# Optimization experiments

Hardware: AMD Instinct MI355X
Metric: run time of the kernel (lower is better)

The kernel has to match this reference:

```python
import jax, jax.numpy as jnp
import numpy as np

B, N, S = 4, 4096, 1024
C1, C2, CO, K = 128, 256, 128, 16
BN_EPS = 1e-5


def setup_inputs() -> dict:
    key = jax.random.key(0)
    ks = jax.random.split(key, 8)
    s = 0.05
    return {
        "xyz1": jax.random.normal(ks[0], (B, N, 3), jnp.float32),
        "xyz2": jax.random.normal(ks[1], (B, S, 3), jnp.float32),
        "points1": jax.random.normal(ks[2], (B, C1, N), jnp.float32),
        "points2": jax.random.normal(ks[3], (B, C2, S), jnp.float32),
        # fuse = ConvBNReLU1D(384 -> 128, k=1)
        "fuse_w": jax.random.normal(ks[4], (CO, C1 + C2), jnp.float32) * s,
        "fuse_b": jnp.zeros((CO,), jnp.float32),
        "fuse_gamma": jnp.ones((CO,), jnp.float32),
        "fuse_beta": jnp.zeros((CO,), jnp.float32),
        # LaplacianUnit conv1x1 (128 -> 128) + BN
        "lu_w": jax.random.normal(ks[5], (CO, CO), jnp.float32) * s,
        "lu_b": jnp.zeros((CO,), jnp.float32),
        "lu_gamma": jnp.ones((CO,), jnp.float32),
        "lu_beta": jnp.zeros((CO,), jnp.float32),
    }


def _sqdist(a, b):
    # a: [B,N,3], b: [B,M,3] -> [B,N,M] squared euclidean distance
    return ((a * a).sum(-1)[:, :, None] + (b * b).sum(-1)[:, None, :]
            - 2.0 * jnp.einsum("bnc,bmc->bnm", a, b))


def _batchnorm1d(x, gamma, beta):
    # x: [B,C,N], training-mode BN (batch statistics, biased variance)
    mean = x.mean(axis=(0, 2), keepdims=True)
    var = ((x - mean) ** 2).mean(axis=(0, 2), keepdims=True)
    xn = (x - mean) * jax.lax.rsqrt(var + BN_EPS)
    return xn * gamma[None, :, None] + beta[None, :, None]


def _gather_points(pts, idx):
    # pts: [B,M,C], idx: [B,N,k] int -> [B,N,k,C]
    return jax.vmap(lambda p, i: p[i])(pts, idx)


def _forward(xyz1, xyz2, points1, points2,
             fuse_w, fuse_b, fuse_gamma, fuse_beta,
             lu_w, lu_b, lu_gamma, lu_beta):
    p2 = jnp.swapaxes(points2, 1, 2)  # [B,S,C2]
    # --- 3-point interpolation (note: torch code uses topk default largest=True) ---
    dists = _sqdist(xyz1, xyz2)                    # [B,N,S]
    top_d, idx = jax.lax.top_k(dists, 3)           # largest, descending (faithful)
    dist_recip = 1.0 / (top_d + 1e-8)
    weight = dist_recip / dist_recip.sum(axis=2, keepdims=True)  # [B,N,3]
    interp = (_gather_points(p2, idx) * weight[..., None]).sum(axis=2)  # [B,N,C2]
    # --- concat skip + fuse conv1x1 + BN + ReLU ---
    new_pts = jnp.concatenate([jnp.swapaxes(points1, 1, 2), interp], axis=-1)  # [B,N,C1+C2]
    x = jnp.einsum("oc,bnc->bon", fuse_w, new_pts) + fuse_b[None, :, None]     # [B,CO,N]
    x = jax.nn.relu(_batchnorm1d(x, fuse_gamma, fuse_beta))
    # --- LaplacianUnit: KNN(k=16) neighbor-sum minus self ---
    d_self = _sqdist(xyz1, xyz1)                   # [B,N,N]
    _, knn_idx = jax.lax.top_k(-d_self, K)         # k smallest distances -> [B,N,K]
    xt = jnp.swapaxes(x, 1, 2)                     # [B,N,CO]
    nbr_sum = _gather_points(xt, knn_idx).sum(axis=2)  # [B,N,CO]
    dx = jnp.swapaxes(nbr_sum, 1, 2) - x           # [B,CO,N]
    h = jnp.einsum("oc,bcn->bon", lu_w, dx) + lu_b[None, :, None]
    h = _batchnorm1d(jax.nn.relu(h), lu_gamma, lu_beta)  # bn(relu(conv(dx))), faithful order
    return x + h


def reference(xyz1, xyz2, points1, points2,
              fuse_w, fuse_b, fuse_gamma, fuse_beta,
              lu_w, lu_b, lu_gamma, lu_beta):
    return _forward(xyz1, xyz2, points1, points2,
                    fuse_w, fuse_b, fuse_gamma, fuse_beta,
                    lu_w, lu_b, lu_gamma, lu_beta)
```

## Files before the change

### kernel.cpp

```cpp
#include <hip/hip_runtime.h>
#include <cfloat>

#define NB 4
#define NN 4096
#define NS 1024
#define NC1 128
#define NC2 256
#define NCO 128
#define NCC 384
#define NK 16
#define KCHUNK 2048
#define KCAP 160
#define KPAD 161


__device__ __forceinline__ float norm3_np(float x, float y, float z) {
  return __fadd_rn(__fadd_rn(__fmul_rn(x, x), __fmul_rn(y, y)), __fmul_rn(z, z));
}

__device__ __forceinline__ float sqdist_np(float nq, float ns,
                                           float qx, float qy, float qz,
                                           float sx, float sy, float sz) {
  float dot = __fadd_rn(__fadd_rn(__fmul_rn(qx, sx), __fmul_rn(qy, sy)),
                        __fmul_rn(qz, sz));
  return __fsub_rn(__fadd_rn(nq, ns), __fmul_rn(2.0f, dot));
}

__global__ void transpose_k(const float* __restrict__ in, float* __restrict__ out,
                            int rows_in, int cols_in, long in_bs, long out_bs, int out_rs) {
  __shared__ float tile[32][33];
  const int b = blockIdx.z;
  const int c0 = blockIdx.x * 32, r0 = blockIdx.y * 32;
  const float* ib = in + (long)b * in_bs;
  float* ob = out + (long)b * out_bs;
#pragma unroll
  for (int k = 0; k < 32; k += 8) {
    tile[threadIdx.y + k][threadIdx.x] =
        ib[(long)(r0 + threadIdx.y + k) * cols_in + c0 + threadIdx.x];
  }
  __syncthreads();
#pragma unroll
  for (int k = 0; k < 32; k += 8) {
    ob[(long)(c0 + threadIdx.y + k) * out_rs + (r0 + threadIdx.x)] =
        tile[threadIdx.x][threadIdx.y + k];
  }
}

__global__ __launch_bounds__(256) void interp_top3_k(const float* __restrict__ xyz1,
                                                     const float* __restrict__ xyz2,
                                                     float* __restrict__ wW,
                                                     int* __restrict__ wIdx) {
  __shared__ float sx[NS], sy[NS], sz[NS], sn[NS];
  __shared__ float md[256 * 3];
  __shared__ int mi[256 * 3];
  const int b = blockIdx.y;
  const int tid = threadIdx.x;
  for (int i = tid; i < NS; i += 256) {
    long base = ((long)b * NS + i) * 3;
    float x = xyz2[base], y = xyz2[base + 1], z = xyz2[base + 2];
    sx[i] = x; sy[i] = y; sz[i] = z;
    sn[i] = norm3_np(x, y, z);
  }
  __syncthreads();
  const int q = (blockIdx.x << 5) + (tid >> 3);
  const int lane = tid & 7;
  long qb = ((long)b * NN + q) * 3;
  const float qx = xyz1[qb], qy = xyz1[qb + 1], qz = xyz1[qb + 2];
  const float nq = norm3_np(qx, qy, qz);
  float bd[3] = {-FLT_MAX, -FLT_MAX, -FLT_MAX};
  int bi[3] = {0x7fffffff, 0x7fffffff, 0x7fffffff};
  for (int s = lane; s < NS; s += 8) {
    float d = sqdist_np(nq, sn[s], qx, qy, qz, sx[s], sy[s], sz[s]);
    if (d > bd[2]) {
      float cd = d; int ci = s;
#pragma unroll
      for (int j = 0; j < 3; ++j) {
        bool gt = cd > bd[j];
        float f = fmaxf(cd, bd[j]);
        float bk = fminf(cd, bd[j]);
        int fi = gt ? ci : bi[j];
        int ki = gt ? bi[j] : ci;
        bd[j] = f; bi[j] = fi; cd = bk; ci = ki;
      }
    }
  }
#pragma unroll
  for (int j = 0; j < 3; ++j) { md[tid * 3 + j] = bd[j]; mi[tid * 3 + j] = bi[j]; }
  __syncthreads();
  if (lane == 0) {
    int p0 = 0, p1 = 0, p2 = 0, p3 = 0, p4 = 0, p5 = 0, p6 = 0, p7 = 0;
    float od[3]; int oi[3];
#pragma unroll
    for (int j = 0; j < 3; ++j) {
      float bv = -FLT_MAX; int bidx = 0x7fffffff; int bl = 0;
#define ITOP_CAND(l, pl)                                                     \
      {                                                                      \
        float t = (pl < 3) ? md[(tid + l) * 3 + pl] : -FLT_MAX;              \
        int ti = (pl < 3) ? mi[(tid + l) * 3 + pl] : 0x7fffffff;             \
        if (t > bv || (t == bv && ti < bidx)) { bv = t; bidx = ti; bl = l; } \
      }
      ITOP_CAND(0, p0) ITOP_CAND(1, p1) ITOP_CAND(2, p2) ITOP_CAND(3, p3)
      ITOP_CAND(4, p4) ITOP_CAND(5, p5) ITOP_CAND(6, p6) ITOP_CAND(7, p7)
#undef ITOP_CAND
      od[j] = bv; oi[j] = bidx;
      p0 += (bl == 0); p1 += (bl == 1); p2 += (bl == 2); p3 += (bl == 3);
      p4 += (bl == 4); p5 += (bl == 5); p6 += (bl == 6); p7 += (bl == 7);
    }
    float r0 = 1.f / (od[0] + 1e-8f);
    float r1 = 1.f / (od[1] + 1e-8f);
    float r2 = 1.f / (od[2] + 1e-8f);
    float sR = __fadd_rn(__fadd_rn(r0, r1), r2);
    long obase = ((long)b * NN + q) * 3;
    wW[obase + 0] = r0 / sR; wW[obase + 1] = r1 / sR; wW[obase + 2] = r2 / sR;
    wIdx[obase + 0] = oi[0]; wIdx[obase + 1] = oi[1]; wIdx[obase + 2] = oi[2];
  }
}

__global__ __launch_bounds__(256) void interp_fill_k(const float* __restrict__ p2t,
                                                     const float* __restrict__ wW,
                                                     const int* __restrict__ wIdx,
                                                     float* __restrict__ nt) {
  const int q = (blockIdx.x << 1) + (threadIdx.x >> 7);
  const int co = threadIdx.x & 127;
  const int b = q >> 12;
  long wb = (long)q * 3;
  float w0 = wW[wb], w1 = wW[wb + 1], w2 = wW[wb + 2];
  int i0 = wIdx[wb], i1 = wIdx[wb + 1], i2 = wIdx[wb + 2];
  const float* r0 = p2t + ((long)(b << 10) + i0) * NC2;
  const float* r1 = p2t + ((long)(b << 10) + i1) * NC2;
  const float* r2 = p2t + ((long)(b << 10) + i2) * NC2;
  float* orow = nt + (long)q * NCC + NC1;
#pragma unroll
  for (int h = 0; h < 2; ++h) {
    int c = co + 128 * h;
    orow[c] = w0 * r0[c] + w1 * r1[c] + w2 * r2[c];
  }
}

template <int C>
__global__ __launch_bounds__(256) void gemm_bias_k(const float* __restrict__ feat,
                                                   const float* __restrict__ W,
                                                   const float* __restrict__ bias,
                                                   float* __restrict__ out) {
  __shared__ float fL[64][36];
  __shared__ float wL[64][36];
  const int r0 = blockIdx.x * 64;
  const int ob = blockIdx.y * 64;
  const int tid = threadIdx.x;
  const int tn = tid & 15;
  const int to = tid >> 4;
  float acc[4][4];
#pragma unroll
  for (int i = 0; i < 4; ++i)
#pragma unroll
    for (int j = 0; j < 4; ++j) acc[i][j] = 0.f;

  for (int c0 = 0; c0 < C; c0 += 32) {
#pragma unroll
    for (int k = 0; k < 8; ++k) {
      int e = tid + 256 * k;
      int rr = e >> 5, cc = e & 31;
      fL[rr][cc] = feat[(long)(r0 + rr) * C + c0 + cc];
    }
#pragma unroll
    for (int k = 0; k < 8; ++k) {
      int e = tid + 256 * k;
      int rr = e >> 5, cc = e & 31;
      wL[rr][cc] = W[(long)(ob + rr) * C + c0 + cc];
    }
    __syncthreads();
#pragma unroll
    for (int cc4 = 0; cc4 < 32; cc4 += 4) {
      float4 fv[4], wv[4];
#pragma unroll
      for (int i = 0; i < 4; ++i) fv[i] = *(const float4*)&fL[tn + 16 * i][cc4];
#pragma unroll
      for (int j = 0; j < 4; ++j) wv[j] = *(const float4*)&wL[to + 16 * j][cc4];
#pragma unroll
      for (int i = 0; i < 4; ++i)
#pragma unroll
        for (int j = 0; j < 4; ++j) {
          acc[i][j] += fv[i].x * wv[j].x + fv[i].y * wv[j].y +
                       fv[i].z * wv[j].z + fv[i].w * wv[j].w;
        }
    }
    __syncthreads();
  }
  const int b = r0 >> 12;
  const int n0 = r0 & 4095;
#pragma unroll
  for (int i = 0; i < 4; ++i) {
    int n = n0 + tn + 16 * i;
#pragma unroll
    for (int j = 0; j < 4; ++j) {
      int o = ob + to + 16 * j;
      out[((long)(b * NCO + o) << 12) + n] = acc[i][j] + bias[o];
    }
  }
}

__global__ __launch_bounds__(256) void bn_stats_k(const float* __restrict__ v,
                                                  const float* __restrict__ gamma,
                                                  const float* __restrict__ beta,
                                                  float* __restrict__ stats, int relu_in) {
  __shared__ float rs[256], rq[256];
  const int o = blockIdx.x, tid = threadIdx.x;
  float s = 0.f, ss = 0.f;
  for (int i = tid; i < NB * NN; i += 256) {
    int b = i >> 12, n = i & 4095;
    float val = v[(((long)b * NCO + o) << 12) + n];
    if (relu_in) val = fmaxf(val, 0.f);
    s += val;
    ss += val * val;
  }
  rs[tid] = s; rq[tid] = ss;
  __syncthreads();
  for (int off = 128; off > 0; off >>= 1) {
    if (tid < off) { rs[tid] += rs[tid + off]; rq[tid] += rq[tid + off]; }
    __syncthreads();
  }
  if (tid == 0) {
    float m = rs[0] * (1.f / 16384.f);
    float var = rq[0] * (1.f / 16384.f) - m * m;
    var = fmaxf(var, 0.f);
    float inv = rsqrtf(var + 1e-5f);
    stats[o] = m;
    stats[128 + o] = inv * gamma[o];
    stats[256 + o] = beta[o];
  }
}

__global__ void fuse_apply_k(const float* __restrict__ xp, const float* __restrict__ stats,
                             float* __restrict__ x, float* __restrict__ xt) {
  __shared__ float tile[32][33];
  const int b = blockIdx.z;
  const int n0 = blockIdx.x * 32;
  const int o0 = blockIdx.y * 32;
  const int tx = threadIdx.x, ty = threadIdx.y;
#pragma unroll
  for (int k = 0; k < 32; k += 8) {
    int o = o0 + ty + k;
    long idx = (((long)b * NCO + o) << 12) + n0 + tx;
    float v = (xp[idx] - stats[o]) * stats[128 + o] + stats[256 + o];
    v = fmaxf(v, 0.f);
    x[idx] = v;
    tile[ty + k][tx] = v;
  }
  __syncthreads();
#pragma unroll
  for (int k = 0; k < 32; k += 8) {
    int n = n0 + ty + k;
    xt[((long)(b << 12) + n) * NCO + o0 + tx] = tile[tx][ty + k];
  }
}

__global__ __launch_bounds__(256) void knn_k(const float* __restrict__ xyz1,
                                             int* __restrict__ knn) {
  __shared__ float4 sc[KCHUNK];
  __shared__ float bufd[32][KPAD];
  __shared__ int bufi[32][KPAD];
  const int b = blockIdx.y;
  const int tid = threadIdx.x;
  const int ql = tid >> 3;
  const int q = (blockIdx.x << 5) + ql;
  const int lane = tid & 7;
  const int gb = (tid & 63) - lane;
  const long qb = ((long)b * NN + q) * 3;
  const float qx = xyz1[qb], qy = xyz1[qb + 1], qz = xyz1[qb + 2];
  const float nq = norm3_np(qx, qy, qz);

  float ta0 = FLT_MAX, ta1 = FLT_MAX, tb0 = FLT_MAX, tb1 = FLT_MAX;
  float tc0 = FLT_MAX, tc1 = FLT_MAX, td0 = FLT_MAX, td1 = FLT_MAX;
  for (int ch = 0; ch < 2; ++ch) {
    for (int i = tid; i < KCHUNK; i += 256) {
      long base = ((long)b * NN + ch * KCHUNK + i) * 3;
      float x = xyz1[base], y = xyz1[base + 1], z = xyz1[base + 2];
      sc[i] = make_float4(x, y, z, norm3_np(x, y, z));
    }
    __syncthreads();
    for (int i = lane; i < KCHUNK; i += 32) {
      float4 v0 = sc[i], v1 = sc[i + 8], v2 = sc[i + 16], v3 = sc[i + 24];
      float d0 = sqdist_np(nq, v0.w, qx, qy, qz, v0.x, v0.y, v0.z);
      float d1 = sqdist_np(nq, v1.w, qx, qy, qz, v1.x, v1.y, v1.z);
      float d2 = sqdist_np(nq, v2.w, qx, qy, qz, v2.x, v2.y, v2.z);
      float d3 = sqdist_np(nq, v3.w, qx, qy, qz, v3.x, v3.y, v3.z);
      float h0 = fmaxf(d0, ta0); ta0 = fminf(d0, ta0); ta1 = fminf(h0, ta1);
      float h1 = fmaxf(d1, tb0); tb0 = fminf(d1, tb0); tb1 = fminf(h1, tb1);
      float h2 = fmaxf(d2, tc0); tc0 = fminf(d2, tc0); tc1 = fminf(h2, tc1);
      float h3 = fmaxf(d3, td0); td0 = fminf(d3, td0); td1 = fminf(h3, td1);
    }
    __syncthreads();
  }
  float m1 = fminf(fminf(ta0, tb0), fminf(tc0, td0));
  float s0 = (ta0 == m1) ? ta1 : ta0;
  float s1 = (tb0 == m1) ? tb1 : tb0;
  float s2 = (tc0 == m1) ? tc1 : tc0;
  float s3 = (td0 == m1) ? td1 : td0;
  float tau = fminf(fminf(s0, s1), fminf(s2, s3));
  tau = fmaxf(tau, __shfl_xor(tau, 1, 64));
  tau = fmaxf(tau, __shfl_xor(tau, 2, 64));
  tau = fmaxf(tau, __shfl_xor(tau, 4, 64));

  int mycnt = 0;
  for (int ch = 0; ch < 2; ++ch) {
    for (int i = tid; i < KCHUNK; i += 256) {
      long base = ((long)b * NN + ch * KCHUNK + i) * 3;
      float x = xyz1[base], y = xyz1[base + 1], z = xyz1[base + 2];
      sc[i] = make_float4(x, y, z, norm3_np(x, y, z));
    }
    __syncthreads();
    const int cb = ch * KCHUNK;
    for (int i = lane; i < KCHUNK; i += 32) {
      float4 v0 = sc[i], v1 = sc[i + 8], v2 = sc[i + 16], v3 = sc[i + 24];
      float d0 = sqdist_np(nq, v0.w, qx, qy, qz, v0.x, v0.y, v0.z);
      float d1 = sqdist_np(nq, v1.w, qx, qy, qz, v1.x, v1.y, v1.z);
      float d2 = sqdist_np(nq, v2.w, qx, qy, qz, v2.x, v2.y, v2.z);
      float d3 = sqdist_np(nq, v3.w, qx, qy, qz, v3.x, v3.y, v3.z);
      bool sv0 = (d0 <= tau), sv1 = (d1 <= tau), sv2 = (d2 <= tau), sv3 = (d3 <= tau);
      unsigned long long m0 = __ballot(sv0);
      unsigned long long m1b = __ballot(sv1);
      unsigned long long m2 = __ballot(sv2);
      unsigned long long m3 = __ballot(sv3);
      unsigned g0 = (unsigned)((m0 >> gb) & 0xFFull);
      unsigned g1 = (unsigned)((m1b >> gb) & 0xFFull);
      unsigned g2 = (unsigned)((m2 >> gb) & 0xFFull);
      unsigned g3 = (unsigned)((m3 >> gb) & 0xFFull);
      unsigned below = (1u << lane) - 1u;
      int c0p = __popc(g0), c1p = __popc(g1), c2p = __popc(g2);
      if (sv0) {
        int pos = mycnt + __popc(g0 & below);
        if (pos < KCAP) { bufd[ql][pos] = d0; bufi[ql][pos] = cb + i; }
      }
      if (sv1) {
        int pos = mycnt + c0p + __popc(g1 & below);
        if (pos < KCAP) { bufd[ql][pos] = d1; bufi[ql][pos] = cb + i + 8; }
      }
      if (sv2) {
        int pos = mycnt + c0p + c1p + __popc(g2 & below);
        if (pos < KCAP) { bufd[ql][pos] = d2; bufi[ql][pos] = cb + i + 16; }
      }
      if (sv3) {
        int pos = mycnt + c0p + c1p + c2p + __popc(g3 & below);
        if (pos < KCAP) { bufd[ql][pos] = d3; bufi[ql][pos] = cb + i + 24; }
      }
      mycnt += c0p + c1p + c2p + __popc(g3);
    }
    __syncthreads();
  }

  float bd[NK]; int bi[NK];
#pragma unroll
  for (int j = 0; j < NK; ++j) { bd[j] = FLT_MAX; bi[j] = 0x7fffffff; }
  if (mycnt > KCAP) {
    for (int s = lane; s < NN; s += 8) {
      long base = ((long)b * NN + s) * 3;
      float x = xyz1[base], y = xyz1[base + 1], z = xyz1[base + 2];
      float d = sqdist_np(nq, norm3_np(x, y, z), qx, qy, qz, x, y, z);
      if (d <= tau) {
        float cd = d; int ci = s;
#pragma unroll
        for (int j = 0; j < NK; ++j) {
          bool lt = cd < bd[j];
          float dmin = fminf(cd, bd[j]);
          float dmax = fmaxf(cd, bd[j]);
          int imin = lt ? ci : bi[j];
          int imax = lt ? bi[j] : ci;
          bd[j] = dmin; bi[j] = imin; cd = dmax; ci = imax;
        }
      }
    }
  } else {
    for (int j0 = lane; j0 < mycnt; j0 += 8) {
      float cd = bufd[ql][j0]; int ci = bufi[ql][j0];
#pragma unroll
      for (int j = 0; j < NK; ++j) {
        bool lt = (cd < bd[j]) || (cd == bd[j] && ci < bi[j]);
        float nd = lt ? cd : bd[j];
        float xd = lt ? bd[j] : cd;
        int ni = lt ? ci : bi[j];
        int xi = lt ? bi[j] : ci;
        bd[j] = nd; bi[j] = ni; cd = xd; ci = xi;
      }
    }
  }
  __syncthreads();

  float* md = (float*)sc;
  int* mi = (int*)sc + 4096;
#pragma unroll
  for (int j = 0; j < NK; ++j) { md[tid * NK + j] = bd[j]; mi[tid * NK + j] = bi[j]; }
  __syncthreads();
  if (lane == 0) {
    int p0 = 0, p1 = 0, p2 = 0, p3 = 0, p4 = 0, p5 = 0, p6 = 0, p7 = 0;
    long obase = ((long)b * NN + q) * NK;
    for (int j = 0; j < NK; ++j) {
      float bv = FLT_MAX; int bidx = 0x7fffffff; int bl = 0;
#define KNN_CAND(l, pl)                                                      \
      {                                                                      \
        float t = (pl < NK) ? md[(tid + l) * NK + pl] : FLT_MAX;             \
        int ti = (pl < NK) ? mi[(tid + l) * NK + pl] : 0x7fffffff;           \
        if (t < bv || (t == bv && ti < bidx)) { bv = t; bidx = ti; bl = l; } \
      }
      KNN_CAND(0, p0) KNN_CAND(1, p1) KNN_CAND(2, p2) KNN_CAND(3, p3)
      KNN_CAND(4, p4) KNN_CAND(5, p5) KNN_CAND(6, p6) KNN_CAND(7, p7)
#undef KNN_CAND
      knn[obase + j] = bidx;
      p0 += (bl == 0); p1 += (bl == 1); p2 += (bl == 2); p3 += (bl == 3);
      p4 += (bl == 4); p5 += (bl == 5); p6 += (bl == 6); p7 += (bl == 7);
    }
  }
}

__global__ __launch_bounds__(256) void lap_gather_k(const float* __restrict__ xt,
                                                    const int* __restrict__ knn,
                                                    float* __restrict__ dxt) {
  const int q = (blockIdx.x << 1) + (threadIdx.x >> 7);
  const int o = threadIdx.x & 127;
  const int b = q >> 12;
  const int* kid = knn + (long)q * NK;
  const long bb = ((long)b << 12) * NCO;
  float s = 0.f;
#pragma unroll
  for (int k = 0; k < NK; ++k) {
    int m = kid[k];
    s += xt[bb + (long)m * NCO + o];
  }
  dxt[(long)q * NCO + o] = s - xt[(long)q * NCO + o];
}

__global__ void final_k(const float* __restrict__ x, const float* __restrict__ hp,
                        const float* __restrict__ stats, float* __restrict__ out) {
  const int stride = gridDim.x * blockDim.x;
  for (int idx = blockIdx.x * blockDim.x + threadIdx.x; idx < NB * NCO * NN; idx += stride) {
    int o = (idx >> 12) & 127;
    float r = fmaxf(hp[idx], 0.f);
    out[idx] = x[idx] + (r - stats[o]) * stats[128 + o] + stats[256 + o];
  }
}

extern "C" void kernel_launch(void* const* d_in, const int* in_sizes, int n_in,
                              void* d_out, int out_size, void* d_ws, size_t ws_size,
                              hipStream_t stream) {
  const float* xyz1 = (const float*)d_in[0];
  const float* xyz2 = (const float*)d_in[1];
  const float* points1 = (const float*)d_in[2];
  const float* points2 = (const float*)d_in[3];
  const float* fuse_w = (const float*)d_in[4];
  const float* fuse_b = (const float*)d_in[5];
  const float* fuse_g = (const float*)d_in[6];
  const float* fuse_be = (const float*)d_in[7];
  const float* lu_w = (const float*)d_in[8];
  const float* lu_b = (const float*)d_in[9];
  const float* lu_g = (const float*)d_in[10];
  const float* lu_be = (const float*)d_in[11];
  (void)in_sizes; (void)n_in; (void)out_size; (void)ws_size;

  char* ws = (char*)d_ws;
  float* p2t = (float*)(ws);
  float* wW = (float*)(ws + 4194304);
  int* wIdx = (int*)(ws + 4390912);
  float* st1 = (float*)(ws + 4587520);
  float* st2 = (float*)(ws + 4589056);
  int* knn = (int*)(ws + 4590592);
  float* nt = (float*)(ws + 5639168);
  float* xp = (float*)(ws + 30804992);
  float* x = (float*)(ws + 39193600);
  float* xt = nt;
  float* dxt = nt + 2097152;
  float* hp = nt + 4194304;

  dim3 tb(32, 8);
  transpose_k<<<dim3(32, 8, NB), tb, 0, stream>>>(points2, p2t, 256, 1024, 262144L, 262144L, 256);
  transpose_k<<<dim3(128, 4, NB), tb, 0, stream>>>(points1, nt, 128, 4096, 524288L, 1572864L, 384);
  interp_top3_k<<<dim3(128, NB), 256, 0, stream>>>(xyz1, xyz2, wW, wIdx);
  interp_fill_k<<<8192, 256, 0, stream>>>(p2t, wW, wIdx, nt);
  gemm_bias_k<NCC><<<dim3(256, 2), 256, 0, stream>>>(nt, fuse_w, fuse_b, xp);
  bn_stats_k<<<128, 256, 0, stream>>>(xp, fuse_g, fuse_be, st1, 0);
  fuse_apply_k<<<dim3(128, 4, NB), tb, 0, stream>>>(xp, st1, x, xt);
  knn_k<<<dim3(128, NB), 256, 0, stream>>>(xyz1, knn);
  lap_gather_k<<<8192, 256, 0, stream>>>(xt, knn, dxt);
  gemm_bias_k<NCO><<<dim3(256, 2), 256, 0, stream>>>(dxt, lu_w, lu_b, hp);
  bn_stats_k<<<128, 256, 0, stream>>>(hp, lu_g, lu_be, st2, 1);
  final_k<<<2048, 256, 0, stream>>>(x, hp, st2, (float*)d_out);
}
```

Baseline: 258.6 us.

## Derive KNN threshold from first chunk only and reuse staged chunk

The KNN kernel now computes its pruning threshold tau from the first 2048 points only, instead of making a full pass over all 4096. The chunk already staged in shared memory is then reused directly for candidate collection. This drops one global staging load and one distance sweep per block. The cost is a looser threshold, so more candidates survive; the candidate buffer capacity is raised to absorb them, which increases shared memory use and may lower occupancy or send more queries to the slow overflow path.

```diff
diff --git a/kernel.cpp b/kernel.cpp
--- a/kernel.cpp
+++ b/kernel.cpp
@@ -10,8 +10,8 @@
 #define NCC 384
 #define NK 16
 #define KCHUNK 2048
-#define KCAP 160
-#define KPAD 161
+#define KCAP 184
+#define KPAD 185
 
 
 __device__ __forceinline__ float norm3_np(float x, float y, float z) {
@@ -269,27 +269,25 @@
   const float qx = xyz1[qb], qy = xyz1[qb + 1], qz = xyz1[qb + 2];
   const float nq = norm3_np(qx, qy, qz);
 
+  for (int i = tid; i < KCHUNK; i += 256) {
+    long base = ((long)b * NN + i) * 3;
+    float x = xyz1[base], y = xyz1[base + 1], z = xyz1[base + 2];
+    sc[i] = make_float4(x, y, z, norm3_np(x, y, z));
+  }
+  __syncthreads();
+
   float ta0 = FLT_MAX, ta1 = FLT_MAX, tb0 = FLT_MAX, tb1 = FLT_MAX;
   float tc0 = FLT_MAX, tc1 = FLT_MAX, td0 = FLT_MAX, td1 = FLT_MAX;
-  for (int ch = 0; ch < 2; ++ch) {
-    for (int i = tid; i < KCHUNK; i += 256) {
-      long base = ((long)b * NN + ch * KCHUNK + i) * 3;
-      float x = xyz1[base], y = xyz1[base + 1], z = xyz1[base + 2];
-      sc[i] = make_float4(x, y, z, norm3_np(x, y, z));
-    }
-    __syncthreads();
-    for (int i = lane; i < KCHUNK; i += 32) {
-      float4 v0 = sc[i], v1 = sc[i + 8], v2 = sc[i + 16], v3 = sc[i + 24];
-      float d0 = sqdist_np(nq, v0.w, qx, qy, qz, v0.x, v0.y, v0.z);
-      float d1 = sqdist_np(nq, v1.w, qx, qy, qz, v1.x, v1.y, v1.z);
-      float d2 = sqdist_np(nq, v2.w, qx, qy, qz, v2.x, v2.y, v2.z);
-      float d3 = sqdist_np(nq, v3.w, qx, qy, qz, v3.x, v3.y, v3.z);
-      float h0 = fmaxf(d0, ta0); ta0 = fminf(d0, ta0); ta1 = fminf(h0, ta1);
-      float h1 = fmaxf(d1, tb0); tb0 = fminf(d1, tb0); tb1 = fminf(h1, tb1);
-      float h2 = fmaxf(d2, tc0); tc0 = fminf(d2, tc0); tc1 = fminf(h2, tc1);
-      float h3 = fmaxf(d3, td0); td0 = fminf(d3, td0); td1 = fminf(h3, td1);
-    }
-    __syncthreads();
+  for (int i = lane; i < KCHUNK; i += 32) {
+    float4 v0 = sc[i], v1 = sc[i + 8], v2 = sc[i + 16], v3 = sc[i + 24];
+    float d0 = sqdist_np(nq, v0.w, qx, qy, qz, v0.x, v0.y, v0.z);
+    float d1 = sqdist_np(nq, v1.w, qx, qy, qz, v1.x, v1.y, v1.z);
+    float d2 = sqdist_np(nq, v2.w, qx, qy, qz, v2.x, v2.y, v2.z);
+    float d3 = sqdist_np(nq, v3.w, qx, qy, qz, v3.x, v3.y, v3.z);
+    float h0 = fmaxf(d0, ta0); ta0 = fminf(d0, ta0); ta1 = fminf(h0, ta1);
+    float h1 = fmaxf(d1, tb0); tb0 = fminf(d1, tb0); tb1 = fminf(h1, tb1);
+    float h2 = fmaxf(d2, tc0); tc0 = fminf(d2, tc0); tc1 = fminf(h2, tc1);
+    float h3 = fmaxf(d3, td0); td0 = fminf(d3, td0); td1 = fminf(h3, td1);
   }
   float m1 = fminf(fminf(ta0, tb0), fminf(tc0, td0));
   float s0 = (ta0 == m1) ? ta1 : ta0;
@@ -302,51 +300,84 @@
   tau = fmaxf(tau, __shfl_xor(tau, 4, 64));
 
   int mycnt = 0;
-  for (int ch = 0; ch < 2; ++ch) {
-    for (int i = tid; i < KCHUNK; i += 256) {
-      long base = ((long)b * NN + ch * KCHUNK + i) * 3;
-      float x = xyz1[base], y = xyz1[base + 1], z = xyz1[base + 2];
-      sc[i] = make_float4(x, y, z, norm3_np(x, y, z));
-    }
-    __syncthreads();
-    const int cb = ch * KCHUNK;
-    for (int i = lane; i < KCHUNK; i += 32) {
-      float4 v0 = sc[i], v1 = sc[i + 8], v2 = sc[i + 16], v3 = sc[i + 24];
-      float d0 = sqdist_np(nq, v0.w, qx, qy, qz, v0.x, v0.y, v0.z);
-      float d1 = sqdist_np(nq, v1.w, qx, qy, qz, v1.x, v1.y, v1.z);
-      float d2 = sqdist_np(nq, v2.w, qx, qy, qz, v2.x, v2.y, v2.z);
-      float d3 = sqdist_np(nq, v3.w, qx, qy, qz, v3.x, v3.y, v3.z);
-      bool sv0 = (d0 <= tau), sv1 = (d1 <= tau), sv2 = (d2 <= tau), sv3 = (d3 <= tau);
-      unsigned long long m0 = __ballot(sv0);
-      unsigned long long m1b = __ballot(sv1);
-      unsigned long long m2 = __ballot(sv2);
-      unsigned long long m3 = __ballot(sv3);
-      unsigned g0 = (unsigned)((m0 >> gb) & 0xFFull);
-      unsigned g1 = (unsigned)((m1b >> gb) & 0xFFull);
-      unsigned g2 = (unsigned)((m2 >> gb) & 0xFFull);
-      unsigned g3 = (unsigned)((m3 >> gb) & 0xFFull);
-      unsigned below = (1u << lane) - 1u;
-      int c0p = __popc(g0), c1p = __popc(g1), c2p = __popc(g2);
-      if (sv0) {
-        int pos = mycnt + __popc(g0 & below);
-        if (pos < KCAP) { bufd[ql][pos] = d0; bufi[ql][pos] = cb + i; }
-      }
-      if (sv1) {
-        int pos = mycnt + c0p + __popc(g1 & below);
-        if (pos < KCAP) { bufd[ql][pos] = d1; bufi[ql][pos] = cb + i + 8; }
-      }
-      if (sv2) {
-        int pos = mycnt + c0p + c1p + __popc(g2 & below);
-        if (pos < KCAP) { bufd[ql][pos] = d2; bufi[ql][pos] = cb + i + 16; }
-      }
-      if (sv3) {
-        int pos = mycnt + c0p + c1p + c2p + __popc(g3 & below);
-        if (pos < KCAP) { bufd[ql][pos] = d3; bufi[ql][pos] = cb + i + 24; }
-      }
-      mycnt += c0p + c1p + c2p + __popc(g3);
-    }
-    __syncthreads();
-  }
+  unsigned below = (1u << lane) - 1u;
+  for (int i = lane; i < KCHUNK; i += 32) {
+    float4 v0 = sc[i], v1 = sc[i + 8], v2 = sc[i + 16], v3 = sc[i + 24];
+    float d0 = sqdist_np(nq, v0.w, qx, qy, qz, v0.x, v0.y, v0.z);
+    float d1 = sqdist_np(nq, v1.w, qx, qy, qz, v1.x, v1.y, v1.z);
+    float d2 = sqdist_np(nq, v2.w, qx, qy, qz, v2.x, v2.y, v2.z);
+    float d3 = sqdist_np(nq, v3.w, qx, qy, qz, v3.x, v3.y, v3.z);
+    bool sv0 = (d0 <= tau), sv1 = (d1 <= tau), sv2 = (d2 <= tau), sv3 = (d3 <= tau);
+    unsigned long long m0 = __ballot(sv0);
+    unsigned long long m1b = __ballot(sv1);
+    unsigned long long m2 = __ballot(sv2);
+    unsigned long long m3 = __ballot(sv3);
+    unsigned g0 = (unsigned)((m0 >> gb) & 0xFFull);
+    unsigned g1 = (unsigned)((m1b >> gb) & 0xFFull);
+    unsigned g2 = (unsigned)((m2 >> gb) & 0xFFull);
+    unsigned g3 = (unsigned)((m3 >> gb) & 0xFFull);
+    int c0p = __popc(g0), c1p = __popc(g1), c2p = __popc(g2);
+    if (sv0) {
+      int pos = mycnt + __popc(g0 & below);
+      if (pos < KCAP) { bufd[ql][pos] = d0; bufi[ql][pos] = i; }
+    }
+    if (sv1) {
+      int pos = mycnt + c0p + __popc(g1 & below);
+      if (pos < KCAP) { bufd[ql][pos] = d1; bufi[ql][pos] = i + 8; }
+    }
+    if (sv2) {
+      int pos = mycnt + c0p + c1p + __popc(g2 & below);
+      if (pos < KCAP) { bufd[ql][pos] = d2; bufi[ql][pos] = i + 16; }
+    }
+    if (sv3) {
+      int pos = mycnt + c0p + c1p + c2p + __popc(g3 & below);
+      if (pos < KCAP) { bufd[ql][pos] = d3; bufi[ql][pos] = i + 24; }
+    }
+    mycnt += c0p + c1p + c2p + __popc(g3);
+  }
+  __syncthreads();
+
+  for (int i = tid; i < KCHUNK; i += 256) {
+    long base = ((long)b * NN + KCHUNK + i) * 3;
+    float x = xyz1[base], y = xyz1[base + 1], z = xyz1[base + 2];
+    sc[i] = make_float4(x, y, z, norm3_np(x, y, z));
+  }
+  __syncthreads();
+  for (int i = lane; i < KCHUNK; i += 32) {
+    float4 v0 = sc[i], v1 = sc[i + 8], v2 = sc[i + 16], v3 = sc[i + 24];
+    float d0 = sqdist_np(nq, v0.w, qx, qy, qz, v0.x, v0.y, v0.z);
+    float d1 = sqdist_np(nq, v1.w, qx, qy, qz, v1.x, v1.y, v1.z);
+    float d2 = sqdist_np(nq, v2.w, qx, qy, qz, v2.x, v2.y, v2.z);
+    float d3 = sqdist_np(nq, v3.w, qx, qy, qz, v3.x, v3.y, v3.z);
+    bool sv0 = (d0 <= tau), sv1 = (d1 <= tau), sv2 = (d2 <= tau), sv3 = (d3 <= tau);
+    unsigned long long m0 = __ballot(sv0);
+    unsigned long long m1b = __ballot(sv1);
+    unsigned long long m2 = __ballot(sv2);
+    unsigned long long m3 = __ballot(sv3);
+    unsigned g0 = (unsigned)((m0 >> gb) & 0xFFull);
+    unsigned g1 = (unsigned)((m1b >> gb) & 0xFFull);
+    unsigned g2 = (unsigned)((m2 >> gb) & 0xFFull);
+    unsigned g3 = (unsigned)((m3 >> gb) & 0xFFull);
+    int c0p = __popc(g0), c1p = __popc(g1), c2p = __popc(g2);
+    if (sv0) {
+      int pos = mycnt + __popc(g0 & below);
+      if (pos < KCAP) { bufd[ql][pos] = d0; bufi[ql][pos] = KCHUNK + i; }
+    }
+    if (sv1) {
+      int pos = mycnt + c0p + __popc(g1 & below);
+      if (pos < KCAP) { bufd[ql][pos] = d1; bufi[ql][pos] = KCHUNK + i + 8; }
+    }
+    if (sv2) {
+      int pos = mycnt + c0p + c1p + __popc(g2 & below);
+      if (pos < KCAP) { bufd[ql][pos] = d2; bufi[ql][pos] = KCHUNK + i + 16; }
+    }
+    if (sv3) {
+      int pos = mycnt + c0p + c1p + c2p + __popc(g3 & below);
+      if (pos < KCAP) { bufd[ql][pos] = d3; bufi[ql][pos] = KCHUNK + i + 24; }
+    }
+    mycnt += c0p + c1p + c2p + __popc(g3);
+  }
+  __syncthreads();
 
   float bd[NK]; int bi[NK];
 #pragma unroll
```

Result: slower. 369.8 us (+43.0%).
